# Kernel optimization log

Hardware: AMD Instinct MI355X
Metric: run time of the kernel (lower is better)

## Reference

```python
import jax, jax.numpy as jnp
import numpy as np

H, K, V = 8, 64, 192   # heads, key_size, value_size
T = 2048               # sequence length
C = H * V              # model dim = 1536
F = 32                 # num_position_features (borzoi central mask, 2 components)


def pos_features_borzoi(positions, feature_size, seq_length):
    # Borzoi central-mask basis, asymmetric (sign-split) version.
    num_basis = feature_size // 2
    pow_rate = np.exp(np.log(seq_length + 1) / num_basis).astype(np.float32)
    center_widths = pow_rate ** jnp.arange(1, num_basis + 1, dtype=jnp.float32) - 1.0  # [nb]
    emb = (center_widths[None, :] > jnp.abs(positions)[:, None]).astype(jnp.float32)   # [2T-1, nb]
    return jnp.concatenate([emb, jnp.sign(positions)[:, None] * emb], axis=-1)         # [2T-1, F]


def relative_shift(x):
    # x: [B, H, T, 2T-1] -> [B, H, T, T]
    b, h, t1, t2 = x.shape
    x = jnp.pad(x, ((0, 0), (0, 0), (0, 0), (1, 0)))   # [B,H,T,2T]
    x = x.reshape(b, h, t2 + 1, t1)[:, :, 1:, :]        # [B,H,2T-1,T]
    x = x.reshape(b, h, t1, t2)
    return x[..., : (t2 + 2) // 2]                      # [B,H,T,T]


def setup_inputs() -> dict:
    key = jax.random.key(0)
    ks = jax.random.split(key, 9)
    s = 0.02
    return {
        'x': jax.random.normal(ks[0], (1, T, C), dtype=jnp.float32),
        'Wq': jax.random.normal(ks[1], (C, H * K), dtype=jnp.float32) * s,
        'Wk': jax.random.normal(ks[2], (C, H * K), dtype=jnp.float32) * s,
        'Wv': jax.random.normal(ks[3], (C, H * V), dtype=jnp.float32) * s,
        'Wr': jax.random.normal(ks[4], (F, H * K), dtype=jnp.float32) * s,
        'r_w_bias': jax.random.normal(ks[5], (1, H, 1, K), dtype=jnp.float32) * s,
        'r_r_bias': jax.random.normal(ks[6], (1, H, 1, K), dtype=jnp.float32) * s,
        'Wo': jax.random.normal(ks[7], (H * V, H * V), dtype=jnp.float32) * s,
        'bo': jnp.zeros((H * V,), dtype=jnp.float32),
    }


def reference(x, Wq, Wk, Wv, Wr, r_w_bias, r_r_bias, Wo, bo):
    B, Tq, _ = x.shape
    q = (x @ Wq).reshape(B, Tq, H, K).transpose(0, 2, 1, 3)  # [B,H,T,K]
    k = (x @ Wk).reshape(B, Tq, H, K).transpose(0, 2, 1, 3)
    v = (x @ Wv).reshape(B, Tq, H, V).transpose(0, 2, 1, 3)  # [B,H,T,V]
    q = q * (K ** -0.5)  # scaling

    # content logits with learned content bias r_w_bias
    content = jnp.einsum('bhqk,bhnk->bhqn', q + r_w_bias, k)  # [B,H,T,T]

    # relative position logits
    distances = jnp.arange(-Tq + 1, Tq, dtype=jnp.float32)    # [2T-1]
    pos_f = pos_features_borzoi(distances, F, Tq)              # [2T-1, F]
    r_k = (pos_f @ Wr).reshape(2 * Tq - 1, H, K)               # [2T-1,H,K]
    rel = jnp.einsum('bhqk,nhk->bhqn', q + r_r_bias, r_k)      # [B,H,T,2T-1]
    rel = relative_shift(rel)                                  # [B,H,T,T]

    attn = jax.nn.softmax(content + rel, axis=-1)
    out = jnp.einsum('bhqn,bhnv->bhqv', attn, v)               # [B,H,T,V]
    out = out.transpose(0, 2, 1, 3).reshape(B, Tq, H * V)      # [B,T,C]
    return out @ Wo + bo
```

## Files before the change

kernel.cpp:

```cpp
#include <hip/hip_runtime.h>
#include <hip/hip_bf16.h>

typedef unsigned short u16;
typedef unsigned int u32;
typedef __bf16 bf16_t;
typedef bf16_t bf16x8 __attribute__((ext_vector_type(8)));
typedef float fx4 __attribute__((ext_vector_type(4)));

#define TT 2048
#define HH 8
#define KK 64
#define VV 192
#define CC 1536
#define SPLITS 3
#define LOG2E 1.4426950408889634f

__device__ __forceinline__ float bf2f(u16 b) {
  union { u32 u; float f; } v; v.u = ((u32)b) << 16; return v.f;
}
__device__ __forceinline__ u16 f2bf(float f) {
  union { float f; u32 u; } v; v.f = f;
  return (u16)((v.u + 0x7FFFu + ((v.u >> 16) & 1u)) >> 16);
}
__device__ __forceinline__ fx4 mfma16(bf16x8 a, bf16x8 b, fx4 c) {
  return __builtin_amdgcn_mfma_f32_16x16x32_bf16(a, b, c, 0, 0, 0);
}
__device__ __forceinline__ void gl_lds16(const u16* g, u16* l) {
  __builtin_amdgcn_global_load_lds(
      (const __attribute__((address_space(1))) u32*)g,
      (__attribute__((address_space(3))) u32*)l, 16, 0, 0);
}

__global__ __launch_bounds__(256) void prep_kernel(
    const float* __restrict__ Wq, const float* __restrict__ Wk,
    const float* __restrict__ Wv, const float* __restrict__ Wo,
    const float* __restrict__ x, const float* __restrict__ Wr,
    const float* __restrict__ rwb, const float* __restrict__ rrb,
    u16* __restrict__ WqT, u16* __restrict__ WkT,
    u16* __restrict__ WvT, u16* __restrict__ WoT,
    u16* __restrict__ xbf, unsigned char* __restrict__ cidx_g,
    u16* __restrict__ WrT, float* __restrict__ dW) {
  const int z = blockIdx.z;
  const int t = threadIdx.x;
  if (z == 4) {
    if (blockIdx.x != 0 || blockIdx.y != 0) return;
    float pr = expf(logf((float)(TT + 1)) / 16.0f);
    float cw[16];
    float wv = pr;
    for (int i = 0; i < 16; ++i) { cw[i] = wv - 1.0f; wv *= pr; }
    for (int idx = t; idx < TT; idx += 256) {
      int c = 15;
      for (int i = 14; i >= 0; --i)
        if (cw[i] > (float)idx) c = i;
      cidx_g[idx] = (unsigned char)c;
    }
    for (int idx = t; idx < 8 * 32 * 64; idx += 256) {
      int hh = idx >> 11, rem = idx & 2047;
      int i = rem >> 6, k = rem & 63;
      WrT[idx] = f2bf(Wr[i * 512 + hh * 64 + k]);
    }
    {
      int hh = t >> 5, i = t & 31;
      float s = 0.0f;
      for (int k = 0; k < 64; ++k)
        s += (rrb[hh * 64 + k] - rwb[hh * 64 + k]) * Wr[i * 512 + hh * 64 + k];
      dW[t] = s * LOG2E;
    }
    return;
  }
  if (z == 5) {
    const size_t ngroups = (size_t)TT * CC / 8;
    int bid = blockIdx.y * 24 + blockIdx.x;
    for (size_t g = (size_t)bid * 256 + t; g < ngroups; g += (size_t)576 * 256) {
      size_t i = g * 8;
      float4 f0 = *(const float4*)&x[i];
      float4 f1 = *(const float4*)&x[i + 4];
      union { u16 h[8]; uint4 v; } pk;
      pk.h[0] = f2bf(f0.x); pk.h[1] = f2bf(f0.y);
      pk.h[2] = f2bf(f0.z); pk.h[3] = f2bf(f0.w);
      pk.h[4] = f2bf(f1.x); pk.h[5] = f2bf(f1.y);
      pk.h[6] = f2bf(f1.z); pk.h[7] = f2bf(f1.w);
      *(uint4*)&xbf[i] = pk.v;
    }
    return;
  }
  if (z < 2 && blockIdx.x >= 8) return;
  const float* in = (z == 0) ? Wq : (z == 1) ? Wk : (z == 2) ? Wv : Wo;
  u16* out = (z == 0) ? WqT : (z == 1) ? WkT : (z == 2) ? WvT : WoT;
  const int in_rs = (z < 2) ? 512 : 1536;
  const int out_rs = 1536;

  __shared__ u16 tile[64][68];
  const int c0 = blockIdx.x * 64, r0 = blockIdx.y * 64;
#pragma unroll
  for (int i = 0; i < 4; ++i) {
    int idx = i * 256 + t;
    int r = idx >> 4, ch = idx & 15;
    float4 fv = *(const float4*)&in[(size_t)(r0 + r) * in_rs + c0 + ch * 4];
    tile[r][ch * 4 + 0] = f2bf(fv.x);
    tile[r][ch * 4 + 1] = f2bf(fv.y);
    tile[r][ch * 4 + 2] = f2bf(fv.z);
    tile[r][ch * 4 + 3] = f2bf(fv.w);
  }
  __syncthreads();
#pragma unroll
  for (int i = 0; i < 4; ++i) {
    int idx = i * 256 + t;
    int r = idx >> 4, ch = idx & 15;
    u16 a0 = tile[ch * 4 + 0][r], a1 = tile[ch * 4 + 1][r];
    u16 a2 = tile[ch * 4 + 2][r], a3 = tile[ch * 4 + 3][r];
    uint2 d;
    d.x = (u32)a0 | ((u32)a1 << 16);
    d.y = (u32)a2 | ((u32)a3 << 16);
    *(uint2*)&out[(size_t)(c0 + r) * out_rs + r0 + ch * 4] = d;
  }
}

__global__ __launch_bounds__(256) void gemm_qkv(
    const u16* __restrict__ xbf, const u16* __restrict__ WqT,
    const u16* __restrict__ WkT, const u16* __restrict__ WvT,
    u16* __restrict__ qw, u16* __restrict__ Kws, u16* __restrict__ vTw,
    const float* __restrict__ rwb) {
  __shared__ u16 As[128 * 64];
  __shared__ u16 Bs[128 * 64];
  const int cb = blockIdx.x;
  const u16* BT = (cb < 4) ? WqT : (cb < 8) ? WkT : WvT;
  const int n0 = ((cb < 4) ? cb : (cb < 8) ? cb - 4 : cb - 8) * 128;
  const int t = threadIdx.x;
  const int lane = t & 63, wid = t >> 6;
  const int l16 = lane & 15, quad = lane >> 4;
  const int wm = wid >> 1, wn = wid & 1;
  const int m0 = blockIdx.y * 128;
  const int wbase = (t & ~63) * 8;

  fx4 acc[4][4] = {};
  for (int k0 = 0; k0 < CC; k0 += 64) {
    __syncthreads();
#pragma unroll
    for (int i = 0; i < 4; ++i) {
      int chunk = i * 256 + t;
      int r = chunk >> 3, ko = (chunk & 7) << 3;
      gl_lds16(&xbf[(size_t)(m0 + r) * CC + k0 + ko], &As[i * 2048 + wbase]);
      gl_lds16(&BT[(size_t)(n0 + r) * CC + k0 + ko], &Bs[i * 2048 + wbase]);
    }
    asm volatile("s_waitcnt vmcnt(0)" ::: "memory");
    __syncthreads();
#pragma unroll
    for (int ks = 0; ks < 2; ++ks) {
      bf16x8 af[4], bfr[4];
#pragma unroll
      for (int mi = 0; mi < 4; ++mi)
        af[mi] = *(const bf16x8*)&As[(wm * 64 + mi * 16 + l16) * 64 + ks * 32 + quad * 8];
#pragma unroll
      for (int ni = 0; ni < 4; ++ni)
        bfr[ni] = *(const bf16x8*)&Bs[(wn * 64 + ni * 16 + l16) * 64 + ks * 32 + quad * 8];
#pragma unroll
      for (int mi = 0; mi < 4; ++mi)
#pragma unroll
        for (int ni = 0; ni < 4; ++ni)
          acc[mi][ni] = mfma16(af[mi], bfr[ni], acc[mi][ni]);
    }
  }

#pragma unroll
  for (int mi = 0; mi < 4; ++mi)
#pragma unroll
    for (int ni = 0; ni < 4; ++ni) {
      int col = n0 + wn * 64 + ni * 16 + l16;
      int row0 = m0 + wm * 64 + mi * 16 + quad * 4;
      if (cb < 8) {
        int h = col >> 6, kx = col & 63;
#pragma unroll
        for (int r = 0; r < 4; ++r) {
          float v = acc[mi][ni][r];
          size_t o = ((size_t)h * TT + row0 + r) * 64 + kx;
          if (cb < 4) qw[o] = f2bf((v * 0.125f + rwb[col]) * LOG2E);
          else Kws[o] = f2bf(v);
        }
      } else {
        int h = col / 192, vv = col - h * 192;
        union { u16 h4[4]; uint2 v2; } pk;
#pragma unroll
        for (int r = 0; r < 4; ++r) pk.h4[r] = f2bf(acc[mi][ni][r]);
        *(uint2*)&vTw[(size_t)h * VV * TT + (size_t)vv * TT + row0] = pk.v2;
      }
    }
}

__global__ __launch_bounds__(256) void gemm_out(
    const u16* __restrict__ A, const u16* __restrict__ BT,
    float* __restrict__ out0, const float* __restrict__ bias0) {
  __shared__ u16 As[128 * 64];
  __shared__ u16 Bs[128 * 64];
  const int t = threadIdx.x;
  const int lane = t & 63, wid = t >> 6;
  const int l16 = lane & 15, quad = lane >> 4;
  const int wm = wid >> 1, wn = wid & 1;
  const int m0 = blockIdx.y * 128, n0 = blockIdx.x * 128;
  const int wbase = (t & ~63) * 8;

  fx4 acc[4][4] = {};
  for (int k0 = 0; k0 < CC; k0 += 64) {
    __syncthreads();
#pragma unroll
    for (int i = 0; i < 4; ++i) {
      int chunk = i * 256 + t;
      int r = chunk >> 3, ko = (chunk & 7) << 3;
      gl_lds16(&A[(size_t)(m0 + r) * CC + k0 + ko], &As[i * 2048 + wbase]);
      gl_lds16(&BT[(size_t)(n0 + r) * CC + k0 + ko], &Bs[i * 2048 + wbase]);
    }
    asm volatile("s_waitcnt vmcnt(0)" ::: "memory");
    __syncthreads();
#pragma unroll
    for (int ks = 0; ks < 2; ++ks) {
      bf16x8 af[4], bfr[4];
#pragma unroll
      for (int mi = 0; mi < 4; ++mi)
        af[mi] = *(const bf16x8*)&As[(wm * 64 + mi * 16 + l16) * 64 + ks * 32 + quad * 8];
#pragma unroll
      for (int ni = 0; ni < 4; ++ni)
        bfr[ni] = *(const bf16x8*)&Bs[(wn * 64 + ni * 16 + l16) * 64 + ks * 32 + quad * 8];
#pragma unroll
      for (int mi = 0; mi < 4; ++mi)
#pragma unroll
        for (int ni = 0; ni < 4; ++ni)
          acc[mi][ni] = mfma16(af[mi], bfr[ni], acc[mi][ni]);
    }
  }
#pragma unroll
  for (int mi = 0; mi < 4; ++mi)
#pragma unroll
    for (int ni = 0; ni < 4; ++ni)
#pragma unroll
      for (int r = 0; r < 4; ++r) {
        int row = m0 + wm * 64 + mi * 16 + quad * 4 + r;
        int col = n0 + wn * 64 + ni * 16 + l16;
        out0[(size_t)row * CC + col] = acc[mi][ni][r] + bias0[col];
      }
}

__global__ __launch_bounds__(256, 3) void attn_split(
    const u16* __restrict__ qw, const u16* __restrict__ Kw,
    const u16* __restrict__ vT, const u16* __restrict__ WrT,
    const float* __restrict__ dW, const unsigned char* __restrict__ cidx_g,
    u16* __restrict__ o_part, float* __restrict__ m_part,
    float* __restrict__ l_part) {
  const int blk = blockIdx.x;
  const int h = blk & 7;
  const int g = blk >> 3;
  const int ks = g % 3;
  const int q0 = (g / 3) * 64;
  const int t = threadIdx.x;
  const int lane = t & 63, w = t >> 6;
  const int l16 = lane & 15, quad = lane >> 4;

  __shared__ u16 KsL[64 * 64];
  __shared__ u16 VsL[192 * 64];
  __shared__ float2 UW[64][17];
  __shared__ unsigned char cidx[TT];
  __shared__ u16 Pl[4][16 * 72];

  *(uint2*)&cidx[t * 8] = *(const uint2*)&cidx_g[t * 8];

  const int qloc = w * 16 + l16;
  const int q_abs = q0 + qloc;
  const u16* qp = qw + ((size_t)h * TT + q_abs) * 64 + quad * 8;
  const bf16x8 aq0 = *(const bf16x8*)qp;
  const bf16x8 aq1 = *(const bf16x8*)(qp + 32);

  {
    const u16* wrt = WrT + h * 32 * 64;
    bf16x8 wb00 = *(const bf16x8*)&wrt[l16 * 64 + quad * 8];
    bf16x8 wb01 = *(const bf16x8*)&wrt[l16 * 64 + 32 + quad * 8];
    bf16x8 wb10 = *(const bf16x8*)&wrt[(16 + l16) * 64 + quad * 8];
    bf16x8 wb11 = *(const bf16x8*)&wrt[(16 + l16) * 64 + 32 + quad * 8];
    fx4 u0 = {}, u1 = {};
    u0 = mfma16(aq0, wb00, u0); u0 = mfma16(aq1, wb01, u0);
    u1 = mfma16(aq0, wb10, u1); u1 = mfma16(aq1, wb11, u1);
    float dw0 = dW[h * 32 + l16], dw1 = dW[h * 32 + 16 + l16];
    float* u_raw = (float*)&Pl[0][0];
#pragma unroll
    for (int r = 0; r < 4; ++r) {
      int qrow = w * 16 + quad * 4 + r;
      u_raw[qrow * 33 + l16] = u0[r] + dw0;
      u_raw[qrow * 33 + 16 + l16] = u1[r] + dw1;
    }
    __syncthreads();
    if (t < 64) {
      float su = 0.f, sw = 0.f;
      float Uv[16], Wv[16];
#pragma unroll
      for (int c = 15; c >= 0; --c) {
        su += u_raw[t * 33 + c]; Uv[c] = su;
        sw += u_raw[t * 33 + 16 + c]; Wv[c] = sw;
      }
#pragma unroll
      for (int c = 0; c < 16; ++c) UW[t][c] = make_float2(Uv[c], Wv[c]);
    }
  }
  __syncthreads();

  float m_s = -3.0e38f, l_s = 0.0f;
  fx4 o[12] = {};
  const u16* kbase = Kw + (size_t)h * TT * 64;
  const u16* vbase = vT + (size_t)h * VV * TT;
  const int jtab[4] = {0, 704, 1408, 2048};
  const int jbeg = jtab[ks], jfin = jtab[ks + 1];

  for (int j0 = jbeg; j0 < jfin; j0 += 64) {
    __builtin_amdgcn_s_barrier();
#pragma unroll
    for (int i = 0; i < 2; ++i) {
      int chunk = i * 256 + t;
      int j = chunk >> 3, c = (chunk & 7) ^ (j & 7);
      gl_lds16(&kbase[(size_t)(j0 + j) * 64 + c * 8],
               &KsL[(size_t)(i * 256 + w * 64) * 8]);
    }
#pragma unroll
    for (int i = 0; i < 6; ++i) {
      int chunk = i * 256 + t;
      int v = chunk >> 3, c = (chunk & 7) ^ (v & 7);
      gl_lds16(&vbase[(size_t)v * TT + j0 + c * 8],
               &VsL[(size_t)(i * 256 + w * 64) * 8]);
    }
    const int dbase = j0 + quad * 4 - q_abs;
    int cc[16];
#pragma unroll
    for (int jt = 0; jt < 4; ++jt)
#pragma unroll
      for (int r = 0; r < 4; ++r) {
        int d = dbase + jt * 16 + r;
        cc[jt * 4 + r] = cidx[d < 0 ? -d : d];
      }
    float2 uwv[16];
#pragma unroll
    for (int i = 0; i < 16; ++i) uwv[i] = UW[qloc][cc[i]];
    asm volatile("s_waitcnt vmcnt(6)" ::: "memory");
    __builtin_amdgcn_s_barrier();
    __builtin_amdgcn_sched_barrier(0);
    bf16x8 kf[8];
#pragma unroll
    for (int jt = 0; jt < 4; ++jt) {
      int j = jt * 16 + l16;
      kf[jt * 2]     = *(const bf16x8*)&KsL[j * 64 + ((quad) ^ (j & 7)) * 8];
      kf[jt * 2 + 1] = *(const bf16x8*)&KsL[j * 64 + ((quad + 4) ^ (j & 7)) * 8];
    }
    fx4 s[4];
    __builtin_amdgcn_s_setprio(1);
#pragma unroll
    for (int jt = 0; jt < 4; ++jt) {
      fx4 z = {0.f, 0.f, 0.f, 0.f};
      z = mfma16(kf[jt * 2], aq0, z);
      s[jt] = mfma16(kf[jt * 2 + 1], aq1, z);
    }
    __builtin_amdgcn_s_setprio(0);
#pragma unroll
    for (int jt = 0; jt < 4; ++jt)
#pragma unroll
      for (int r = 0; r < 4; ++r) {
        int d = dbase + jt * 16 + r;
        float2 z = uwv[jt * 4 + r];
        s[jt][r] += z.x + (d > 0 ? z.y : (d < 0 ? -z.y : 0.0f));
      }
    float mx = s[0][0];
#pragma unroll
    for (int jt = 0; jt < 4; ++jt)
#pragma unroll
      for (int r = 0; r < 4; ++r) mx = fmaxf(mx, s[jt][r]);
    mx = fmaxf(mx, __shfl_xor(mx, 16, 64));
    mx = fmaxf(mx, __shfl_xor(mx, 32, 64));
    if (!__all(mx - m_s <= 8.0f)) {
      float mnew = fmaxf(m_s, mx);
      float alpha = exp2f(m_s - mnew);
      float a4[4];
#pragma unroll
      for (int r = 0; r < 4; ++r) a4[r] = __shfl(alpha, quad * 4 + r, 16);
#pragma unroll
      for (int vt = 0; vt < 12; ++vt)
#pragma unroll
        for (int r = 0; r < 4; ++r) o[vt][r] *= a4[r];
      l_s *= alpha;
      m_s = mnew;
    }
    float p16[16];
    float ps = 0.0f;
#pragma unroll
    for (int jt = 0; jt < 4; ++jt)
#pragma unroll
      for (int r = 0; r < 4; ++r) {
        float p = exp2f(s[jt][r] - m_s);
        p16[jt * 4 + r] = p;
        ps += p;
      }
    ps += __shfl_xor(ps, 16, 64);
    ps += __shfl_xor(ps, 32, 64);
    l_s += ps;
#pragma unroll
    for (int jt = 0; jt < 4; ++jt) {
      union { u16 h4[4]; uint2 v; } pk;
#pragma unroll
      for (int r = 0; r < 4; ++r) pk.h4[r] = f2bf(p16[jt * 4 + r]);
      *(uint2*)&Pl[w][l16 * 72 + jt * 16 + quad * 4] = pk.v;
    }
    asm volatile("s_waitcnt lgkmcnt(0)" ::: "memory");
    bf16x8 pf0 = *(const bf16x8*)&Pl[w][l16 * 72 + quad * 8];
    bf16x8 pf1 = *(const bf16x8*)&Pl[w][l16 * 72 + 32 + quad * 8];
    asm volatile("s_waitcnt vmcnt(0)" ::: "memory");
    __builtin_amdgcn_s_barrier();
    __builtin_amdgcn_sched_barrier(0);
    __builtin_amdgcn_s_setprio(1);
#pragma unroll
    for (int vt = 0; vt < 12; ++vt) {
      int v = vt * 16 + l16;
      bf16x8 bv = *(const bf16x8*)&VsL[v * 64 + ((quad) ^ (v & 7)) * 8];
      o[vt] = mfma16(pf0, bv, o[vt]);
    }
#pragma unroll
    for (int vt = 0; vt < 12; ++vt) {
      int v = vt * 16 + l16;
      bf16x8 bv = *(const bf16x8*)&VsL[v * 64 + ((quad + 4) ^ (v & 7)) * 8];
      o[vt] = mfma16(pf1, bv, o[vt]);
    }
    __builtin_amdgcn_s_setprio(0);
  }

#pragma unroll
  for (int r = 0; r < 4; ++r) {
    int row = q0 + w * 16 + quad * 4 + r;
    size_t base = ((size_t)(ks * HH + h) * TT + row) * VV;
#pragma unroll
    for (int vt = 0; vt < 12; ++vt) o_part[base + vt * 16 + l16] = f2bf(o[vt][r]);
  }
  if (quad == 0) {
    m_part[(size_t)(ks * HH + h) * TT + q_abs] = m_s;
    l_part[(size_t)(ks * HH + h) * TT + q_abs] = l_s;
  }
}

__global__ __launch_bounds__(256) void attn_combine(
    const u16* __restrict__ o_part, const float* __restrict__ m_part,
    const float* __restrict__ l_part, u16* __restrict__ aout) {
  const int h = blockIdx.y;
  const int row = blockIdx.x * 16 + (threadIdx.x >> 4);
  const int c0 = (threadIdx.x & 15) * 12;

  float m[SPLITS], M = -3.0e38f;
#pragma unroll
  for (int s = 0; s < SPLITS; ++s) {
    m[s] = m_part[(size_t)(s * HH + h) * TT + row];
    M = fmaxf(M, m[s]);
  }
  float lsum = 0.0f, wgt[SPLITS];
#pragma unroll
  for (int s = 0; s < SPLITS; ++s) {
    wgt[s] = exp2f(m[s] - M);
    lsum += wgt[s] * l_part[(size_t)(s * HH + h) * TT + row];
  }
  float o[12];
#pragma unroll
  for (int j = 0; j < 12; ++j) o[j] = 0.0f;
#pragma unroll
  for (int s = 0; s < SPLITS; ++s) {
    const u16* op = o_part + ((size_t)(s * HH + h) * TT + row) * VV + c0;
    float wgts = wgt[s];
    uint2 u0 = *(const uint2*)&op[0];
    uint2 u1 = *(const uint2*)&op[4];
    uint2 u2 = *(const uint2*)&op[8];
    u32 uu[6] = {u0.x, u0.y, u1.x, u1.y, u2.x, u2.y};
#pragma unroll
    for (int j = 0; j < 6; ++j) {
      o[j * 2 + 0] = fmaf(wgts, bf2f((u16)(uu[j] & 0xFFFF)), o[j * 2 + 0]);
      o[j * 2 + 1] = fmaf(wgts, bf2f((u16)(uu[j] >> 16)), o[j * 2 + 1]);
    }
  }
  float inv = 1.0f / lsum;
  union { u16 hx[12]; uint2 v2[3]; } pk;
#pragma unroll
  for (int j = 0; j < 12; ++j) pk.hx[j] = f2bf(o[j] * inv);
  u16* dst = aout + (size_t)row * CC + h * VV + c0;
  *(uint2*)&dst[0] = pk.v2[0];
  *(uint2*)&dst[4] = pk.v2[1];
  *(uint2*)&dst[8] = pk.v2[2];
}

extern "C" void kernel_launch(void* const* d_in, const int* in_sizes, int n_in,
                              void* d_out, int out_size, void* d_ws, size_t ws_size,
                              hipStream_t stream) {
  (void)in_sizes; (void)n_in; (void)out_size; (void)ws_size;
  const float* x   = (const float*)d_in[0];
  const float* Wq  = (const float*)d_in[1];
  const float* Wk  = (const float*)d_in[2];
  const float* Wv  = (const float*)d_in[3];
  const float* Wr  = (const float*)d_in[4];
  const float* rwb = (const float*)d_in[5];
  const float* rrb = (const float*)d_in[6];
  const float* Wo  = (const float*)d_in[7];
  const float* bo  = (const float*)d_in[8];

  char* ws = (char*)d_ws;
  size_t off = 0;
  auto alloc = [&](size_t bytes) -> void* {
    void* p = ws + off;
    off += (bytes + 255) & ~(size_t)255;
    return p;
  };
  u16* WqT  = (u16*)alloc((size_t)512 * 1536 * 2);
  u16* WkT  = (u16*)alloc((size_t)512 * 1536 * 2);
  u16* WvT  = (u16*)alloc((size_t)1536 * 1536 * 2);
  u16* WoT  = (u16*)alloc((size_t)1536 * 1536 * 2);
  u16* xbf  = (u16*)alloc((size_t)TT * CC * 2);
  u16* qw   = (u16*)alloc((size_t)HH * TT * 64 * 2);
  u16* Kws  = (u16*)alloc((size_t)HH * TT * 64 * 2);
  u16* vTw  = (u16*)alloc((size_t)HH * VV * TT * 2);
  u16* aout = (u16*)alloc((size_t)TT * CC * 2);
  unsigned char* cidx_g = (unsigned char*)alloc(TT);
  u16* WrT      = (u16*)alloc((size_t)HH * 32 * 64 * 2);
  float* dW     = (float*)alloc((size_t)HH * 32 * 4);
  u16* o_part   = (u16*)alloc((size_t)SPLITS * HH * TT * VV * 2);
  float* m_part = (float*)alloc((size_t)SPLITS * HH * TT * 4);
  float* l_part = (float*)alloc((size_t)SPLITS * HH * TT * 4);

  prep_kernel<<<dim3(24, 24, 6), 256, 0, stream>>>(
      Wq, Wk, Wv, Wo, x, Wr, rwb, rrb,
      WqT, WkT, WvT, WoT, xbf, cidx_g, WrT, dW);
  gemm_qkv<<<dim3(20, 16), 256, 0, stream>>>(xbf, WqT, WkT, WvT,
                                             qw, Kws, vTw, rwb);
  attn_split<<<dim3(768), 256, 0, stream>>>(qw, Kws, vTw, WrT, dW, cidx_g,
                                            o_part, m_part, l_part);
  attn_combine<<<dim3(128, 8), 256, 0, stream>>>(o_part, m_part, l_part, aout);
  gemm_out<<<dim3(12, 16), 256, 0, stream>>>(aout, WoT, (float*)d_out, bo);
}
```

Baseline: 237.4 us.

## Double-buffer LDS, swizzle layout, and halve N tile in projection GEMMs

Both projection GEMMs (QKV and output) now double-buffer their LDS tiles, so the next K-slice load overlaps the MFMA work on the current one. LDS rows are XOR-swizzled to avoid bank conflicts. The N tile shrinks from 128 to 64 and the grids double, giving more blocks to fill the GPU. In exchange, each block reuses less data per tile, more A-tile loads go to global memory, and the kernels need more shared memory per block.

```diff
diff --git a/kernel.cpp b/kernel.cpp
--- a/kernel.cpp
+++ b/kernel.cpp
@@ -121,60 +121,77 @@
     const u16* __restrict__ WkT, const u16* __restrict__ WvT,
     u16* __restrict__ qw, u16* __restrict__ Kws, u16* __restrict__ vTw,
     const float* __restrict__ rwb) {
-  __shared__ u16 As[128 * 64];
-  __shared__ u16 Bs[128 * 64];
+  __shared__ u16 As[2][128 * 64];
+  __shared__ u16 Bs[2][64 * 64];
   const int cb = blockIdx.x;
-  const u16* BT = (cb < 4) ? WqT : (cb < 8) ? WkT : WvT;
-  const int n0 = ((cb < 4) ? cb : (cb < 8) ? cb - 4 : cb - 8) * 128;
+  const u16* BT = (cb < 8) ? WqT : (cb < 16) ? WkT : WvT;
+  const int n0 = ((cb < 8) ? cb : (cb < 16) ? cb - 8 : cb - 16) * 64;
   const int t = threadIdx.x;
   const int lane = t & 63, wid = t >> 6;
   const int l16 = lane & 15, quad = lane >> 4;
   const int wm = wid >> 1, wn = wid & 1;
   const int m0 = blockIdx.y * 128;
-  const int wbase = (t & ~63) * 8;
-
-  fx4 acc[4][4] = {};
-  for (int k0 = 0; k0 < CC; k0 += 64) {
-    __syncthreads();
+  const int wbase = wid * 512;
+
+  auto stage = [&](int p, int k0) {
 #pragma unroll
     for (int i = 0; i < 4; ++i) {
       int chunk = i * 256 + t;
-      int r = chunk >> 3, ko = (chunk & 7) << 3;
-      gl_lds16(&xbf[(size_t)(m0 + r) * CC + k0 + ko], &As[i * 2048 + wbase]);
-      gl_lds16(&BT[(size_t)(n0 + r) * CC + k0 + ko], &Bs[i * 2048 + wbase]);
+      int r = chunk >> 3, c = (chunk & 7) ^ (r & 7);
+      gl_lds16(&xbf[(size_t)(m0 + r) * CC + k0 + c * 8], &As[p][i * 2048 + wbase]);
+    }
+#pragma unroll
+    for (int i = 0; i < 2; ++i) {
+      int chunk = i * 256 + t;
+      int r = chunk >> 3, c = (chunk & 7) ^ (r & 7);
+      gl_lds16(&BT[(size_t)(n0 + r) * CC + k0 + c * 8], &Bs[p][i * 2048 + wbase]);
+    }
+  };
+
+  fx4 acc[4][2] = {};
+  stage(0, 0);
+  asm volatile("s_waitcnt vmcnt(0)" ::: "memory");
+  __builtin_amdgcn_s_barrier();
+  int p = 0;
+  for (int kt = 0; kt < 24; ++kt) {
+    if (kt != 23) stage(p ^ 1, (kt + 1) * 64);
+#pragma unroll
+    for (int ks = 0; ks < 2; ++ks) {
+      bf16x8 af[4], bfr[2];
+#pragma unroll
+      for (int mi = 0; mi < 4; ++mi) {
+        int Ra = wm * 64 + mi * 16 + l16;
+        af[mi] = *(const bf16x8*)&As[p][Ra * 64 + (((ks * 4 + quad) ^ (Ra & 7))) * 8];
+      }
+#pragma unroll
+      for (int ni = 0; ni < 2; ++ni) {
+        int Rb = wn * 32 + ni * 16 + l16;
+        bfr[ni] = *(const bf16x8*)&Bs[p][Rb * 64 + (((ks * 4 + quad) ^ (Rb & 7))) * 8];
+      }
+#pragma unroll
+      for (int mi = 0; mi < 4; ++mi)
+#pragma unroll
+        for (int ni = 0; ni < 2; ++ni)
+          acc[mi][ni] = mfma16(af[mi], bfr[ni], acc[mi][ni]);
     }
     asm volatile("s_waitcnt vmcnt(0)" ::: "memory");
-    __syncthreads();
-#pragma unroll
-    for (int ks = 0; ks < 2; ++ks) {
-      bf16x8 af[4], bfr[4];
-#pragma unroll
-      for (int mi = 0; mi < 4; ++mi)
-        af[mi] = *(const bf16x8*)&As[(wm * 64 + mi * 16 + l16) * 64 + ks * 32 + quad * 8];
-#pragma unroll
-      for (int ni = 0; ni < 4; ++ni)
-        bfr[ni] = *(const bf16x8*)&Bs[(wn * 64 + ni * 16 + l16) * 64 + ks * 32 + quad * 8];
-#pragma unroll
-      for (int mi = 0; mi < 4; ++mi)
-#pragma unroll
-        for (int ni = 0; ni < 4; ++ni)
-          acc[mi][ni] = mfma16(af[mi], bfr[ni], acc[mi][ni]);
-    }
+    __builtin_amdgcn_s_barrier();
+    p ^= 1;
   }
 
 #pragma unroll
   for (int mi = 0; mi < 4; ++mi)
 #pragma unroll
-    for (int ni = 0; ni < 4; ++ni) {
-      int col = n0 + wn * 64 + ni * 16 + l16;
+    for (int ni = 0; ni < 2; ++ni) {
+      int col = n0 + wn * 32 + ni * 16 + l16;
       int row0 = m0 + wm * 64 + mi * 16 + quad * 4;
-      if (cb < 8) {
+      if (cb < 16) {
         int h = col >> 6, kx = col & 63;
 #pragma unroll
         for (int r = 0; r < 4; ++r) {
           float v = acc[mi][ni][r];
           size_t o = ((size_t)h * TT + row0 + r) * 64 + kx;
-          if (cb < 4) qw[o] = f2bf((v * 0.125f + rwb[col]) * LOG2E);
+          if (cb < 8) qw[o] = f2bf((v * 0.125f + rwb[col]) * LOG2E);
           else Kws[o] = f2bf(v);
         }
       } else {
@@ -190,51 +207,68 @@
 __global__ __launch_bounds__(256) void gemm_out(
     const u16* __restrict__ A, const u16* __restrict__ BT,
     float* __restrict__ out0, const float* __restrict__ bias0) {
-  __shared__ u16 As[128 * 64];
-  __shared__ u16 Bs[128 * 64];
+  __shared__ u16 As[2][128 * 64];
+  __shared__ u16 Bs[2][64 * 64];
   const int t = threadIdx.x;
   const int lane = t & 63, wid = t >> 6;
   const int l16 = lane & 15, quad = lane >> 4;
   const int wm = wid >> 1, wn = wid & 1;
-  const int m0 = blockIdx.y * 128, n0 = blockIdx.x * 128;
-  const int wbase = (t & ~63) * 8;
-
-  fx4 acc[4][4] = {};
-  for (int k0 = 0; k0 < CC; k0 += 64) {
-    __syncthreads();
+  const int m0 = blockIdx.y * 128, n0 = blockIdx.x * 64;
+  const int wbase = wid * 512;
+
+  auto stage = [&](int p, int k0) {
 #pragma unroll
     for (int i = 0; i < 4; ++i) {
       int chunk = i * 256 + t;
-      int r = chunk >> 3, ko = (chunk & 7) << 3;
-      gl_lds16(&A[(size_t)(m0 + r) * CC + k0 + ko], &As[i * 2048 + wbase]);
-      gl_lds16(&BT[(size_t)(n0 + r) * CC + k0 + ko], &Bs[i * 2048 + wbase]);
+      int r = chunk >> 3, c = (chunk & 7) ^ (r & 7);
+      gl_lds16(&A[(size_t)(m0 + r) * CC + k0 + c * 8], &As[p][i * 2048 + wbase]);
+    }
+#pragma unroll
+    for (int i = 0; i < 2; ++i) {
+      int chunk = i * 256 + t;
+      int r = chunk >> 3, c = (chunk & 7) ^ (r & 7);
+      gl_lds16(&BT[(size_t)(n0 + r) * CC + k0 + c * 8], &Bs[p][i * 2048 + wbase]);
+    }
+  };
+
+  fx4 acc[4][2] = {};
+  stage(0, 0);
+  asm volatile("s_waitcnt vmcnt(0)" ::: "memory");
+  __builtin_amdgcn_s_barrier();
+  int p = 0;
+  for (int kt = 0; kt < 24; ++kt) {
+    if (kt != 23) stage(p ^ 1, (kt + 1) * 64);
+#pragma unroll
+    for (int ks = 0; ks < 2; ++ks) {
+      bf16x8 af[4], bfr[2];
+#pragma unroll
+      for (int mi = 0; mi < 4; ++mi) {
+        int Ra = wm * 64 + mi * 16 + l16;
+        af[mi] = *(const bf16x8*)&As[p][Ra * 64 + (((ks * 4 + quad) ^ (Ra & 7))) * 8];
+      }
+#pragma unroll
+      for (int ni = 0; ni < 2; ++ni) {
+        int Rb = wn * 32 + ni * 16 + l16;
+        bfr[ni] = *(const bf16x8*)&Bs[p][Rb * 64 + (((ks * 4 + quad) ^ (Rb & 7))) * 8];
+      }
+#pragma unroll
+      for (int mi = 0; mi < 4; ++mi)
+#pragma unroll
+        for (int ni = 0; ni < 2; ++ni)
+          acc[mi][ni] = mfma16(af[mi], bfr[ni], acc[mi][ni]);
     }
     asm volatile("s_waitcnt vmcnt(0)" ::: "memory");
-    __syncthreads();
-#pragma unroll
-    for (int ks = 0; ks < 2; ++ks) {
-      bf16x8 af[4], bfr[4];
-#pragma unroll
-      for (int mi = 0; mi < 4; ++mi)
-        af[mi] = *(const bf16x8*)&As[(wm * 64 + mi * 16 + l16) * 64 + ks * 32 + quad * 8];
-#pragma unroll
-      for (int ni = 0; ni < 4; ++ni)
-        bfr[ni] = *(const bf16x8*)&Bs[(wn * 64 + ni * 16 + l16) * 64 + ks * 32 + quad * 8];
-#pragma unroll
-      for (int mi = 0; mi < 4; ++mi)
-#pragma unroll
-        for (int ni = 0; ni < 4; ++ni)
-          acc[mi][ni] = mfma16(af[mi], bfr[ni], acc[mi][ni]);
-    }
+    __builtin_amdgcn_s_barrier();
+    p ^= 1;
   }
 #pragma unroll
   for (int mi = 0; mi < 4; ++mi)
 #pragma unroll
-    for (int ni = 0; ni < 4; ++ni)
+    for (int ni = 0; ni < 2; ++ni)
 #pragma unroll
       for (int r = 0; r < 4; ++r) {
         int row = m0 + wm * 64 + mi * 16 + quad * 4 + r;
-        int col = n0 + wn * 64 + ni * 16 + l16;
+        int col = n0 + wn * 32 + ni * 16 + l16;
         out0[(size_t)row * CC + col] = acc[mi][ni][r] + bias0[col];
       }
 }
@@ -523,10 +557,10 @@
   prep_kernel<<<dim3(24, 24, 6), 256, 0, stream>>>(
       Wq, Wk, Wv, Wo, x, Wr, rwb, rrb,
       WqT, WkT, WvT, WoT, xbf, cidx_g, WrT, dW);
-  gemm_qkv<<<dim3(20, 16), 256, 0, stream>>>(xbf, WqT, WkT, WvT,
+  gemm_qkv<<<dim3(40, 16), 256, 0, stream>>>(xbf, WqT, WkT, WvT,
                                              qw, Kws, vTw, rwb);
   attn_split<<<dim3(768), 256, 0, stream>>>(qw, Kws, vTw, WrT, dW, cidx_g,
                                             o_part, m_part, l_part);
   attn_combine<<<dim3(128, 8), 256, 0, stream>>>(o_part, m_part, l_part, aout);
-  gemm_out<<<dim3(12, 16), 256, 0, stream>>>(aout, WoT, (float*)d_out, bo);
-}
+  gemm_out<<<dim3(24, 16), 256, 0, stream>>>(aout, WoT, (float*)d_out, bo);
+}
```

Result: faster. 205.6 us (-13.4%).
